# Kernel tuning notes

Hardware: AMD Instinct MI355X
Metric: run time of the kernel (lower is better)

## Reference

```python
import jax, jax.numpy as jnp
from jax import lax
import numpy as np

H_DIM = 256
BETA = 0.1
BATCH = 32768
N_STEPS = 32
DT = 0.01
GAIN_TANH = 5.0 / 3.0  # nn.init.calculate_gain('tanh')


def _xavier_uniform(key, fan_out, fan_in, gain):
    limit = gain * jnp.sqrt(6.0 / (fan_in + fan_out))
    return jax.random.uniform(key, (fan_out, fan_in), dtype=jnp.float32,
                              minval=-limit, maxval=limit)


def setup_inputs() -> dict:
    key = jax.random.key(0)
    ks = jax.random.split(key, 6)
    t_eval = jnp.arange(N_STEPS, dtype=jnp.float32) * DT
    state0 = 0.1 * jax.random.normal(ks[0], (BATCH, 4), dtype=jnp.float32)
    W1 = _xavier_uniform(ks[1], H_DIM, 4, GAIN_TANH)
    W2 = _xavier_uniform(ks[2], H_DIM, H_DIM, GAIN_TANH)
    W3 = _xavier_uniform(ks[3], H_DIM, H_DIM, GAIN_TANH)
    W4 = _xavier_uniform(ks[4], 1, H_DIM, GAIN_TANH)
    b1 = jnp.zeros((H_DIM,), jnp.float32)
    b2 = jnp.zeros((H_DIM,), jnp.float32)
    b3 = jnp.zeros((H_DIM,), jnp.float32)
    b4 = jnp.zeros((1,), jnp.float32)
    scale = jnp.asarray(0.005, dtype=jnp.float32)
    return {"t_eval": t_eval, "state0": state0,
            "W1": W1, "b1": b1, "W2": W2, "b2": b2,
            "W3": W3, "b3": b3, "W4": W4, "b4": b4, "scale": scale}


def _hamiltonian_sum(s, W1, b1, W2, b2, W3, b3, W4, b4):
    # 4 -> h -> h -> h -> 1 tanh MLP; sum over batch so grad gives per-sample dH/ds
    h = jnp.tanh(s @ W1.T + b1)
    h = jnp.tanh(h @ W2.T + b2)
    h = jnp.tanh(h @ W3.T + b3)
    return jnp.sum(h @ W4.T + b4)


def _verlet_step(state, dt):
    # exact Henon-Heiles velocity-verlet; state: (B, 4) = (q1, p1, q2, p2)
    q1, p1, q2, p2 = state[:, 0], state[:, 1], state[:, 2], state[:, 3]
    F1 = -q1 * (1.0 + 2.0 * q2)
    F2 = -(q2 + q1 ** 2 - q2 ** 2)
    p1h = p1 + 0.5 * dt * F1
    p2h = p2 + 0.5 * dt * F2
    q1n = q1 + dt * p1h
    q2n = q2 + dt * p2h
    F1n = -q1n * (1.0 + 2.0 * q2n)
    F2n = -(q2n + q1n ** 2 - q2n ** 2)
    p1n = p1h + 0.5 * dt * F1n
    p2n = p2h + 0.5 * dt * F2n
    return jnp.stack([q1n, p1n, q2n, p2n], axis=1)


def reference(t_eval, state0, W1, b1, W2, b2, W3, b3, W4, b4, scale):
    dt = t_eval[1] - t_eval[0]
    n_steps = t_eval.shape[0]

    def corr_dyn(state):
        # torch detaches the state before the autograd-Hamiltonian gradient
        s = lax.stop_gradient(state)
        g = jax.grad(_hamiltonian_sum)(s, W1, b1, W2, b2, W3, b3, W4, b4)  # (B,4)
        # symplectic rotation of grad_H: (dq1, dp1, dq2, dp2)
        return jnp.stack([g[:, 1], -g[:, 0], g[:, 3], -g[:, 2]], axis=1)

    def step(state, _):
        corr = corr_dyn(state)
        corr_norm = jnp.linalg.norm(corr, axis=1, keepdims=True)  # (B,1)
        adapt_dt = lax.stop_gradient(
            dt * jnp.clip(1.0 - BETA * corr_norm, 0.5, 1.0))
        new_state = _verlet_step(state, dt) + adapt_dt * (scale * corr)
        return new_state, new_state

    _, traj = lax.scan(step, state0, None, length=n_steps - 1)  # (T-1, B, 4)
    full = jnp.concatenate([state0[None], traj], axis=0)        # (T, B, 4)
    return jnp.transpose(full, (1, 0, 2))                        # (B, T, 4)
```

## Files before the change

kernel.cpp:

```cpp
#include <hip/hip_runtime.h>
#include <hip/hip_bf16.h>
#include <math.h>

#define H       256
#define TB      64
#define NT      512
#define NSTEPS  32
#define XS      264
#define DS1     260

typedef __attribute__((ext_vector_type(8)))  short short8v;
typedef __attribute__((ext_vector_type(16))) float f32x16;

__device__ __forceinline__ float fast_tanh(float x) {
    float e;
    asm("v_exp_f32 %0, %1" : "=v"(e) : "v"(x * 2.8853900817779268f));
    return fmaf(-2.0f, __builtin_amdgcn_rcpf(e + 1.0f), 1.0f);
}

__device__ __forceinline__ unsigned pk2(float lo, float hi) {
    __hip_bfloat162 h2 = __float22bfloat162_rn(make_float2(lo, hi));
    unsigned u; __builtin_memcpy(&u, &h2, 4);
    return u;
}
__device__ __forceinline__ unsigned short f2b(float x) {
    unsigned u = __float_as_uint(x);
    u += 0x7FFFu + ((u >> 16) & 1u);
    return (unsigned short)(u >> 16);
}
__device__ __forceinline__ float b2f(unsigned short h) {
    return __uint_as_float(((unsigned)h) << 16);
}

__global__ void convert_w(const float* __restrict__ W2, const float* __restrict__ W3,
                          unsigned short* __restrict__ wsb) {
    int t = blockIdx.x * blockDim.x + threadIdx.x;
    int i = t >> 8, j = t & 255;
    float w2 = W2[t], w3 = W3[t];
    wsb[t]                         = f2b(w2);
    wsb[65536 + t]                 = f2b(w3);
    wsb[131072 + (j << 8) + i]     = f2b(w2);
    wsb[196608 + (j << 8) + i]     = f2b(w3);
}

#define PREFETCH_W(dst, base)                                                  \
    _Pragma("unroll")                                                          \
    for (int kc = 0; kc < 16; ++kc)                                            \
        dst[kc] = *reinterpret_cast<const short8v*>((base) + kc * 16);         \
    __builtin_amdgcn_sched_barrier(0);

#define MFMA_CHAIN(WREG, XSRC, A0, A1)                                         \
    _Pragma("unroll")                                                          \
    for (int kc = 0; kc < 16; ++kc) {                                          \
        short8v bA = *reinterpret_cast<const short8v*>(&XSRC[col][kc*16 + q*8]);      \
        short8v bB = *reinterpret_cast<const short8v*>(&XSRC[32 + col][kc*16 + q*8]); \
        A0 = __builtin_amdgcn_mfma_f32_32x32x16_bf16(WREG[kc], bA, A0, 0, 0, 0);      \
        A1 = __builtin_amdgcn_mfma_f32_32x32x16_bf16(WREG[kc], bB, A1, 0, 0, 0);      \
    }

__global__ __launch_bounds__(NT, 2)
void sympnet_mfma(const float* __restrict__ t_eval,
                  const float* __restrict__ state0,
                  const float* __restrict__ W1, const float* __restrict__ b1,
                  const float* __restrict__ b2, const float* __restrict__ b3,
                  const float* __restrict__ W4, const float* __restrict__ scale_p,
                  const short* __restrict__ W2b,  const short* __restrict__ W3b,
                  const short* __restrict__ W2Tb, const short* __restrict__ W3Tb,
                  float* __restrict__ out)
{
    __shared__ unsigned short Xa[TB][XS];
    __shared__ unsigned short Xb[TB][XS];
    __shared__ unsigned short D1[TB][DS1];
    __shared__ float sS[TB][4];
    __shared__ float gp[8][TB][4];
    __shared__ float sW1[H * 4];
    __shared__ float sB1[H], sB2[H], sB3[H], sW4[H];

    const int tid  = threadIdx.x;
    const int lane = tid & 63;
    const int wv   = tid >> 6;
    const int col  = lane & 31;
    const int q    = lane >> 5;
    const int n0   = wv * 32;

    const float dt    = t_eval[1] - t_eval[0];
    const float scale = scale_p[0];
    const int   b0    = blockIdx.x * TB;

    const short* W2p  = W2b  + ((n0 + col) << 8) + q * 8;
    const short* W3p  = W3b  + ((n0 + col) << 8) + q * 8;
    const short* W3Tp = W3Tb + ((n0 + col) << 8) + q * 8;
    const short* W2Tp = W2Tb + ((n0 + col) << 8) + q * 8;

    short8v wA[16], wB[16];
    PREFETCH_W(wA, W2p);

    if (tid < H) {
        reinterpret_cast<float4*>(sW1)[tid] = reinterpret_cast<const float4*>(W1)[tid];
        sB1[tid] = b1[tid];
        sB2[tid] = b2[tid];
        sB3[tid] = b3[tid];
        sW4[tid] = W4[tid];
    }
    if (tid < TB) {
        float4 s = reinterpret_cast<const float4*>(state0)[b0 + tid];
        sS[tid][0] = s.x; sS[tid][1] = s.y; sS[tid][2] = s.z; sS[tid][3] = s.w;
        reinterpret_cast<float4*>(out)[(size_t)(b0 + tid) * NSTEPS] = s;
    }
    __syncthreads();

    float d2[32];

    for (int t = 1; t < NSTEPS; ++t) {
        {
            const int j0  = (tid & 31) * 8;
            const int i0v = (tid >> 5) * 4;
            float4 wvv[8];
            #pragma unroll
            for (int jj = 0; jj < 8; ++jj)
                wvv[jj] = reinterpret_cast<const float4*>(sW1)[j0 + jj];
            float bb[8];
            #pragma unroll
            for (int jj = 0; jj < 8; ++jj) bb[jj] = sB1[j0 + jj];
            #pragma unroll
            for (int ii = 0; ii < 4; ++ii) {
                float4 sv = *reinterpret_cast<const float4*>(&sS[i0v + ii][0]);
                float h[8], d[8];
                #pragma unroll
                for (int jj = 0; jj < 8; ++jj) {
                    float z = bb[jj] + sv.x * wvv[jj].x + sv.y * wvv[jj].y
                                     + sv.z * wvv[jj].z + sv.w * wvv[jj].w;
                    h[jj] = fast_tanh(z);
                    d[jj] = fmaf(-h[jj], h[jj], 1.0f);
                }
                *reinterpret_cast<uint2*>(&Xa[i0v + ii][j0]) =
                    make_uint2(pk2(h[0], h[1]), pk2(h[2], h[3]));
                *reinterpret_cast<uint2*>(&Xa[i0v + ii][j0 + 4]) =
                    make_uint2(pk2(h[4], h[5]), pk2(h[6], h[7]));
                *reinterpret_cast<uint2*>(&D1[i0v + ii][j0]) =
                    make_uint2(pk2(d[0], d[1]), pk2(d[2], d[3]));
                *reinterpret_cast<uint2*>(&D1[i0v + ii][j0 + 4]) =
                    make_uint2(pk2(d[4], d[5]), pk2(d[6], d[7]));
            }
        }
        __syncthreads();

        {
            PREFETCH_W(wB, W3p);
            float4 bv4[4];
            #pragma unroll
            for (int g = 0; g < 4; ++g)
                bv4[g] = *reinterpret_cast<const float4*>(&sB2[n0 + 8*g + 4*q]);
            f32x16 acc0 = {}, acc1 = {};
            MFMA_CHAIN(wA, Xa, acc0, acc1);
            #pragma unroll
            for (int mt = 0; mt < 2; ++mt) {
                f32x16 acc = (mt == 0) ? acc0 : acc1;
                #pragma unroll
                for (int g = 0; g < 4; ++g) {
                    const float* bp = reinterpret_cast<const float*>(&bv4[g]);
                    float h[4];
                    #pragma unroll
                    for (int rr = 0; rr < 4; ++rr) {
                        h[rr] = fast_tanh(acc[4*g + rr] + bp[rr]);
                        d2[mt*16 + 4*g + rr] = fmaf(-h[rr], h[rr], 1.0f);
                    }
                    *reinterpret_cast<uint2*>(&Xb[mt*32 + col][n0 + 8*g + 4*q]) =
                        make_uint2(pk2(h[0], h[1]), pk2(h[2], h[3]));
                }
            }
        }
        __syncthreads();

        {
            PREFETCH_W(wA, W3Tp);
            float4 bv4[4], wv4[4];
            #pragma unroll
            for (int g = 0; g < 4; ++g) {
                bv4[g] = *reinterpret_cast<const float4*>(&sB3[n0 + 8*g + 4*q]);
                wv4[g] = *reinterpret_cast<const float4*>(&sW4[n0 + 8*g + 4*q]);
            }
            f32x16 acc0 = {}, acc1 = {};
            MFMA_CHAIN(wB, Xb, acc0, acc1);
            #pragma unroll
            for (int mt = 0; mt < 2; ++mt) {
                f32x16 acc = (mt == 0) ? acc0 : acc1;
                #pragma unroll
                for (int g = 0; g < 4; ++g) {
                    const float* bp = reinterpret_cast<const float*>(&bv4[g]);
                    const float* wp = reinterpret_cast<const float*>(&wv4[g]);
                    float u[4];
                    #pragma unroll
                    for (int rr = 0; rr < 4; ++rr) {
                        float h = fast_tanh(acc[4*g + rr] + bp[rr]);
                        u[rr] = wp[rr] * fmaf(-h, h, 1.0f);
                    }
                    *reinterpret_cast<uint2*>(&Xa[mt*32 + col][n0 + 8*g + 4*q]) =
                        make_uint2(pk2(u[0], u[1]), pk2(u[2], u[3]));
                }
            }
        }
        __syncthreads();

        {
            PREFETCH_W(wB, W2Tp);
            f32x16 acc0 = {}, acc1 = {};
            MFMA_CHAIN(wA, Xa, acc0, acc1);
            #pragma unroll
            for (int mt = 0; mt < 2; ++mt) {
                f32x16 acc = (mt == 0) ? acc0 : acc1;
                #pragma unroll
                for (int g = 0; g < 4; ++g) {
                    float u[4];
                    #pragma unroll
                    for (int rr = 0; rr < 4; ++rr)
                        u[rr] = acc[4*g + rr] * d2[mt*16 + 4*g + rr];
                    *reinterpret_cast<uint2*>(&Xb[mt*32 + col][n0 + 8*g + 4*q]) =
                        make_uint2(pk2(u[0], u[1]), pk2(u[2], u[3]));
                }
            }
        }
        __syncthreads();

        {
            PREFETCH_W(wA, W2p);
            f32x16 acc0 = {}, acc1 = {};
            MFMA_CHAIN(wB, Xb, acc0, acc1);
            float pg[2][4] = {};
            #pragma unroll
            for (int g = 0; g < 4; ++g) {
                float4 w1v[4];
                #pragma unroll
                for (int rr = 0; rr < 4; ++rr)
                    w1v[rr] = reinterpret_cast<const float4*>(sW1)[n0 + 8*g + 4*q + rr];
                #pragma unroll
                for (int mt = 0; mt < 2; ++mt) {
                    f32x16 acc = (mt == 0) ? acc0 : acc1;
                    short4 dv = *reinterpret_cast<const short4*>(&D1[mt*32 + col][n0 + 8*g + 4*q]);
                    float dd[4] = { b2f((unsigned short)dv.x), b2f((unsigned short)dv.y),
                                    b2f((unsigned short)dv.z), b2f((unsigned short)dv.w) };
                    #pragma unroll
                    for (int rr = 0; rr < 4; ++rr) {
                        float u1 = acc[4*g + rr] * dd[rr];
                        float4 w = w1v[rr];
                        pg[mt][0] = fmaf(u1, w.x, pg[mt][0]);
                        pg[mt][1] = fmaf(u1, w.y, pg[mt][1]);
                        pg[mt][2] = fmaf(u1, w.z, pg[mt][2]);
                        pg[mt][3] = fmaf(u1, w.w, pg[mt][3]);
                    }
                }
            }
            #pragma unroll
            for (int mt = 0; mt < 2; ++mt) {
                float p0 = pg[mt][0], p1 = pg[mt][1], p2 = pg[mt][2], p3 = pg[mt][3];
                p0 += __shfl_xor(p0, 32); p1 += __shfl_xor(p1, 32);
                p2 += __shfl_xor(p2, 32); p3 += __shfl_xor(p3, 32);
                if (q == 0)
                    *reinterpret_cast<float4*>(&gp[wv][mt*32 + col][0]) =
                        make_float4(p0, p1, p2, p3);
            }
        }
        __syncthreads();

        if (tid < TB) {
            float g0 = 0.f, g1 = 0.f, g2 = 0.f, g3 = 0.f;
            #pragma unroll
            for (int w = 0; w < 8; ++w) {
                float4 p = *reinterpret_cast<const float4*>(&gp[w][tid][0]);
                g0 += p.x; g1 += p.y; g2 += p.z; g3 += p.w;
            }
            float c0 = g1, c1 = -g0, c2 = g3, c3 = -g2;
            float nrm = sqrtf(c0*c0 + c1*c1 + c2*c2 + c3*c3);
            float ad  = dt * fminf(fmaxf(1.0f - 0.1f * nrm, 0.5f), 1.0f);
            float q1  = sS[tid][0], p1v = sS[tid][1];
            float q2  = sS[tid][2], p2v = sS[tid][3];
            float F1  = -q1 * (1.0f + 2.0f * q2);
            float F2  = -(q2 + q1 * q1 - q2 * q2);
            float p1h = p1v + 0.5f * dt * F1;
            float p2h = p2v + 0.5f * dt * F2;
            float q1n = q1 + dt * p1h;
            float q2n = q2 + dt * p2h;
            float F1n = -q1n * (1.0f + 2.0f * q2n);
            float F2n = -(q2n + q1n * q1n - q2n * q2n);
            float p1n = p1h + 0.5f * dt * F1n;
            float p2n = p2h + 0.5f * dt * F2n;
            float as  = ad * scale;
            float ns0 = q1n + as * c0;
            float ns1 = p1n + as * c1;
            float ns2 = q2n + as * c2;
            float ns3 = p2n + as * c3;
            sS[tid][0] = ns0; sS[tid][1] = ns1; sS[tid][2] = ns2; sS[tid][3] = ns3;
            reinterpret_cast<float4*>(out)[(size_t)(b0 + tid) * NSTEPS + t] =
                make_float4(ns0, ns1, ns2, ns3);
        }
        __syncthreads();
    }
}

extern "C" void kernel_launch(void* const* d_in, const int* in_sizes, int n_in,
                              void* d_out, int out_size, void* d_ws, size_t ws_size,
                              hipStream_t stream) {
    const float* t_eval = (const float*)d_in[0];
    const float* state0 = (const float*)d_in[1];
    const float* W1     = (const float*)d_in[2];
    const float* b1     = (const float*)d_in[3];
    const float* W2     = (const float*)d_in[4];
    const float* b2     = (const float*)d_in[5];
    const float* W3     = (const float*)d_in[6];
    const float* b3     = (const float*)d_in[7];
    const float* W4     = (const float*)d_in[8];
    const float* scale  = (const float*)d_in[10];
    float* out = (float*)d_out;

    unsigned short* wsb = (unsigned short*)d_ws;
    convert_w<<<dim3(256), dim3(256), 0, stream>>>(W2, W3, wsb);

    const short* W2b  = (const short*)(wsb);
    const short* W3b  = (const short*)(wsb + 65536);
    const short* W2Tb = (const short*)(wsb + 131072);
    const short* W3Tb = (const short*)(wsb + 196608);

    const int batch = in_sizes[1] / 4;
    sympnet_mfma<<<dim3(batch / TB), dim3(NT), 0, stream>>>(
        t_eval, state0, W1, b1, b2, b3, W4, scale,
        W2b, W3b, W2Tb, W3Tb, out);
}
```

Measured before the change: 1.213 ms.

## Split batch rows across 16 waves with dual independent MFMA accumulator chains

The block grows from 8 to 16 waves, with each wave now handling one 32-row batch tile instead of two. The MFMA K loop is split into even and odd halves that accumulate into two independent accumulators, which are summed in the epilogue. This keeps two MFMA dependency chains in flight per wave and halves per-wave register state such as d2 and the accumulators. The cost is that each wave still prefetches the full weight slice, so weight register loads are duplicated across twice as many waves, and occupancy drops to one block per CU.

```diff
diff --git a/kernel.cpp b/kernel.cpp
--- a/kernel.cpp
+++ b/kernel.cpp
@@ -4,7 +4,7 @@
 
 #define H       256
 #define TB      64
-#define NT      512
+#define NT      1024
 #define NSTEPS  32
 #define XS      264
 #define DS1     260
@@ -51,14 +51,14 @@
 
 #define MFMA_CHAIN(WREG, XSRC, A0, A1)                                         \
     _Pragma("unroll")                                                          \
-    for (int kc = 0; kc < 16; ++kc) {                                          \
-        short8v bA = *reinterpret_cast<const short8v*>(&XSRC[col][kc*16 + q*8]);      \
-        short8v bB = *reinterpret_cast<const short8v*>(&XSRC[32 + col][kc*16 + q*8]); \
-        A0 = __builtin_amdgcn_mfma_f32_32x32x16_bf16(WREG[kc], bA, A0, 0, 0, 0);      \
-        A1 = __builtin_amdgcn_mfma_f32_32x32x16_bf16(WREG[kc], bB, A1, 0, 0, 0);      \
+    for (int kc = 0; kc < 8; ++kc) {                                           \
+        short8v be = *reinterpret_cast<const short8v*>(&XSRC[mrow][(2*kc)*16 + q*8]);   \
+        short8v bo = *reinterpret_cast<const short8v*>(&XSRC[mrow][(2*kc+1)*16 + q*8]); \
+        A0 = __builtin_amdgcn_mfma_f32_32x32x16_bf16(WREG[2*kc],   be, A0, 0, 0, 0);    \
+        A1 = __builtin_amdgcn_mfma_f32_32x32x16_bf16(WREG[2*kc+1], bo, A1, 0, 0, 0);    \
     }
 
-__global__ __launch_bounds__(NT, 2)
+__global__ __launch_bounds__(NT, 1)
 void sympnet_mfma(const float* __restrict__ t_eval,
                   const float* __restrict__ state0,
                   const float* __restrict__ W1, const float* __restrict__ b1,
@@ -79,9 +79,12 @@
     const int tid  = threadIdx.x;
     const int lane = tid & 63;
     const int wv   = tid >> 6;
+    const int r    = wv & 7;
+    const int mt   = wv >> 3;
     const int col  = lane & 31;
     const int q    = lane >> 5;
-    const int n0   = wv * 32;
+    const int n0   = r * 32;
+    const int mrow = mt * 32 + col;
 
     const float dt    = t_eval[1] - t_eval[0];
     const float scale = scale_p[0];
@@ -109,12 +112,12 @@
     }
     __syncthreads();
 
-    float d2[32];
+    float d2[16];
 
     for (int t = 1; t < NSTEPS; ++t) {
         {
-            const int j0  = (tid & 31) * 8;
-            const int i0v = (tid >> 5) * 4;
+            const int j0 = (tid & 31) * 8;
+            const int r0 = (tid >> 5) * 2;
             float4 wvv[8];
             #pragma unroll
             for (int jj = 0; jj < 8; ++jj)
@@ -123,8 +126,8 @@
             #pragma unroll
             for (int jj = 0; jj < 8; ++jj) bb[jj] = sB1[j0 + jj];
             #pragma unroll
-            for (int ii = 0; ii < 4; ++ii) {
-                float4 sv = *reinterpret_cast<const float4*>(&sS[i0v + ii][0]);
+            for (int ii = 0; ii < 2; ++ii) {
+                float4 sv = *reinterpret_cast<const float4*>(&sS[r0 + ii][0]);
                 float h[8], d[8];
                 #pragma unroll
                 for (int jj = 0; jj < 8; ++jj) {
@@ -133,13 +136,13 @@
                     h[jj] = fast_tanh(z);
                     d[jj] = fmaf(-h[jj], h[jj], 1.0f);
                 }
-                *reinterpret_cast<uint2*>(&Xa[i0v + ii][j0]) =
+                *reinterpret_cast<uint2*>(&Xa[r0 + ii][j0]) =
                     make_uint2(pk2(h[0], h[1]), pk2(h[2], h[3]));
-                *reinterpret_cast<uint2*>(&Xa[i0v + ii][j0 + 4]) =
+                *reinterpret_cast<uint2*>(&Xa[r0 + ii][j0 + 4]) =
                     make_uint2(pk2(h[4], h[5]), pk2(h[6], h[7]));
-                *reinterpret_cast<uint2*>(&D1[i0v + ii][j0]) =
+                *reinterpret_cast<uint2*>(&D1[r0 + ii][j0]) =
                     make_uint2(pk2(d[0], d[1]), pk2(d[2], d[3]));
-                *reinterpret_cast<uint2*>(&D1[i0v + ii][j0 + 4]) =
+                *reinterpret_cast<uint2*>(&D1[r0 + ii][j0 + 4]) =
                     make_uint2(pk2(d[4], d[5]), pk2(d[6], d[7]));
             }
         }
@@ -151,23 +154,19 @@
             #pragma unroll
             for (int g = 0; g < 4; ++g)
                 bv4[g] = *reinterpret_cast<const float4*>(&sB2[n0 + 8*g + 4*q]);
-            f32x16 acc0 = {}, acc1 = {};
-            MFMA_CHAIN(wA, Xa, acc0, acc1);
-            #pragma unroll
-            for (int mt = 0; mt < 2; ++mt) {
-                f32x16 acc = (mt == 0) ? acc0 : acc1;
-                #pragma unroll
-                for (int g = 0; g < 4; ++g) {
-                    const float* bp = reinterpret_cast<const float*>(&bv4[g]);
-                    float h[4];
-                    #pragma unroll
-                    for (int rr = 0; rr < 4; ++rr) {
-                        h[rr] = fast_tanh(acc[4*g + rr] + bp[rr]);
-                        d2[mt*16 + 4*g + rr] = fmaf(-h[rr], h[rr], 1.0f);
-                    }
-                    *reinterpret_cast<uint2*>(&Xb[mt*32 + col][n0 + 8*g + 4*q]) =
-                        make_uint2(pk2(h[0], h[1]), pk2(h[2], h[3]));
+            f32x16 a0 = {}, a1 = {};
+            MFMA_CHAIN(wA, Xa, a0, a1);
+            #pragma unroll
+            for (int g = 0; g < 4; ++g) {
+                const float* bp = reinterpret_cast<const float*>(&bv4[g]);
+                float h[4];
+                #pragma unroll
+                for (int rr = 0; rr < 4; ++rr) {
+                    h[rr] = fast_tanh(a0[4*g + rr] + a1[4*g + rr] + bp[rr]);
+                    d2[4*g + rr] = fmaf(-h[rr], h[rr], 1.0f);
                 }
+                *reinterpret_cast<uint2*>(&Xb[mrow][n0 + 8*g + 4*q]) =
+                    make_uint2(pk2(h[0], h[1]), pk2(h[2], h[3]));
             }
         }
         __syncthreads();
@@ -180,85 +179,67 @@
                 bv4[g] = *reinterpret_cast<const float4*>(&sB3[n0 + 8*g + 4*q]);
                 wv4[g] = *reinterpret_cast<const float4*>(&sW4[n0 + 8*g + 4*q]);
             }
-            f32x16 acc0 = {}, acc1 = {};
-            MFMA_CHAIN(wB, Xb, acc0, acc1);
-            #pragma unroll
-            for (int mt = 0; mt < 2; ++mt) {
-                f32x16 acc = (mt == 0) ? acc0 : acc1;
-                #pragma unroll
-                for (int g = 0; g < 4; ++g) {
-                    const float* bp = reinterpret_cast<const float*>(&bv4[g]);
-                    const float* wp = reinterpret_cast<const float*>(&wv4[g]);
-                    float u[4];
-                    #pragma unroll
-                    for (int rr = 0; rr < 4; ++rr) {
-                        float h = fast_tanh(acc[4*g + rr] + bp[rr]);
-                        u[rr] = wp[rr] * fmaf(-h, h, 1.0f);
-                    }
-                    *reinterpret_cast<uint2*>(&Xa[mt*32 + col][n0 + 8*g + 4*q]) =
-                        make_uint2(pk2(u[0], u[1]), pk2(u[2], u[3]));
+            f32x16 a0 = {}, a1 = {};
+            MFMA_CHAIN(wB, Xb, a0, a1);
+            #pragma unroll
+            for (int g = 0; g < 4; ++g) {
+                const float* bp = reinterpret_cast<const float*>(&bv4[g]);
+                const float* wp = reinterpret_cast<const float*>(&wv4[g]);
+                float u[4];
+                #pragma unroll
+                for (int rr = 0; rr < 4; ++rr) {
+                    float h = fast_tanh(a0[4*g + rr] + a1[4*g + rr] + bp[rr]);
+                    u[rr] = wp[rr] * fmaf(-h, h, 1.0f);
                 }
+                *reinterpret_cast<uint2*>(&Xa[mrow][n0 + 8*g + 4*q]) =
+                    make_uint2(pk2(u[0], u[1]), pk2(u[2], u[3]));
             }
         }
         __syncthreads();
 
         {
             PREFETCH_W(wB, W2Tp);
-            f32x16 acc0 = {}, acc1 = {};
-            MFMA_CHAIN(wA, Xa, acc0, acc1);
-            #pragma unroll
-            for (int mt = 0; mt < 2; ++mt) {
-                f32x16 acc = (mt == 0) ? acc0 : acc1;
-                #pragma unroll
-                for (int g = 0; g < 4; ++g) {
-                    float u[4];
-                    #pragma unroll
-                    for (int rr = 0; rr < 4; ++rr)
-                        u[rr] = acc[4*g + rr] * d2[mt*16 + 4*g + rr];
-                    *reinterpret_cast<uint2*>(&Xb[mt*32 + col][n0 + 8*g + 4*q]) =
-                        make_uint2(pk2(u[0], u[1]), pk2(u[2], u[3]));
-                }
+            f32x16 a0 = {}, a1 = {};
+            MFMA_CHAIN(wA, Xa, a0, a1);
+            #pragma unroll
+            for (int g = 0; g < 4; ++g) {
+                float u[4];
+                #pragma unroll
+                for (int rr = 0; rr < 4; ++rr)
+                    u[rr] = (a0[4*g + rr] + a1[4*g + rr]) * d2[4*g + rr];
+                *reinterpret_cast<uint2*>(&Xb[mrow][n0 + 8*g + 4*q]) =
+                    make_uint2(pk2(u[0], u[1]), pk2(u[2], u[3]));
             }
         }
         __syncthreads();
 
         {
             PREFETCH_W(wA, W2p);
-            f32x16 acc0 = {}, acc1 = {};
-            MFMA_CHAIN(wB, Xb, acc0, acc1);
-            float pg[2][4] = {};
+            f32x16 a0 = {}, a1 = {};
+            MFMA_CHAIN(wB, Xb, a0, a1);
+            float pg0 = 0.f, pg1 = 0.f, pg2 = 0.f, pg3 = 0.f;
             #pragma unroll
             for (int g = 0; g < 4; ++g) {
                 float4 w1v[4];
                 #pragma unroll
                 for (int rr = 0; rr < 4; ++rr)
                     w1v[rr] = reinterpret_cast<const float4*>(sW1)[n0 + 8*g + 4*q + rr];
-                #pragma unroll
-                for (int mt = 0; mt < 2; ++mt) {
-                    f32x16 acc = (mt == 0) ? acc0 : acc1;
-                    short4 dv = *reinterpret_cast<const short4*>(&D1[mt*32 + col][n0 + 8*g + 4*q]);
-                    float dd[4] = { b2f((unsigned short)dv.x), b2f((unsigned short)dv.y),
-                                    b2f((unsigned short)dv.z), b2f((unsigned short)dv.w) };
-                    #pragma unroll
-                    for (int rr = 0; rr < 4; ++rr) {
-                        float u1 = acc[4*g + rr] * dd[rr];
-                        float4 w = w1v[rr];
-                        pg[mt][0] = fmaf(u1, w.x, pg[mt][0]);
-                        pg[mt][1] = fmaf(u1, w.y, pg[mt][1]);
-                        pg[mt][2] = fmaf(u1, w.z, pg[mt][2]);
-                        pg[mt][3] = fmaf(u1, w.w, pg[mt][3]);
-                    }
+                short4 dv = *reinterpret_cast<const short4*>(&D1[mrow][n0 + 8*g + 4*q]);
+                float dd[4] = { b2f((unsigned short)dv.x), b2f((unsigned short)dv.y),
+                                b2f((unsigned short)dv.z), b2f((unsigned short)dv.w) };
+                #pragma unroll
+                for (int rr = 0; rr < 4; ++rr) {
+                    float u1 = (a0[4*g + rr] + a1[4*g + rr]) * dd[rr];
+                    float4 w = w1v[rr];
+                    pg0 = fmaf(u1, w.x, pg0); pg1 = fmaf(u1, w.y, pg1);
+                    pg2 = fmaf(u1, w.z, pg2); pg3 = fmaf(u1, w.w, pg3);
                 }
             }
-            #pragma unroll
-            for (int mt = 0; mt < 2; ++mt) {
-                float p0 = pg[mt][0], p1 = pg[mt][1], p2 = pg[mt][2], p3 = pg[mt][3];
-                p0 += __shfl_xor(p0, 32); p1 += __shfl_xor(p1, 32);
-                p2 += __shfl_xor(p2, 32); p3 += __shfl_xor(p3, 32);
-                if (q == 0)
-                    *reinterpret_cast<float4*>(&gp[wv][mt*32 + col][0]) =
-                        make_float4(p0, p1, p2, p3);
-            }
+            pg0 += __shfl_xor(pg0, 32); pg1 += __shfl_xor(pg1, 32);
+            pg2 += __shfl_xor(pg2, 32); pg3 += __shfl_xor(pg3, 32);
+            if (q == 0)
+                *reinterpret_cast<float4*>(&gp[r][mrow][0]) =
+                    make_float4(pg0, pg1, pg2, pg3);
         }
         __syncthreads();
 
```

Measured after the change: 3.919 ms. +223.0%, slower.
